# Kernel tuning notes

Hardware: AMD Instinct MI355X
Metric: run time of the kernel (lower is better)

Reference implementation:

```python
import jax, jax.numpy as jnp
import numpy as np

N = 2048   # query length
M = 2048   # key length
B = 2      # batch
D = 1024   # model dim (d_x_q = d_x_kv = d_out)
H = 16     # heads
DQK = D // H
DV = D // H
OFFSET = 0


def setup_inputs() -> dict:
    key = jax.random.key(0)
    k1, k2, k3, k4, k5, k6 = jax.random.split(key, 6)
    return {
        "x_q": jax.random.normal(k1, (N, B, D), dtype=jnp.float32),
        "x_kv": jax.random.normal(k2, (M, B, D), dtype=jnp.float32),
        "to_q": jax.random.normal(k3, (H, DQK, D), dtype=jnp.float32),
        "to_kv": jax.random.normal(k4, (H, DQK + DV, D), dtype=jnp.float32),
        "for_pos_enc": jax.random.normal(k5, (H, DQK, D), dtype=jnp.float32),
        "to_o": jax.random.normal(k6, (D, H, DV), dtype=jnp.float32),
    }


def _pos_enc(for_pos_enc, n, m, offset, d_x_kv):
    # relative distances i - j + offset, range [offset-(m-1), offset+(n-1)]
    dmin = offset - (m - 1)
    dmax = offset + (n - 1)
    r = jnp.arange(dmin, dmax + 1, dtype=jnp.float32)            # [R]
    inv_freq = 1.0 / (10000.0 ** (jnp.arange(0.0, d_x_kv, 2.0, dtype=jnp.float32) / d_x_kv))
    phases = r[:, None] * inv_freq[None, :]                       # [R, d/2]
    sincos = jnp.concatenate([jnp.sin(phases), jnp.cos(phases)], axis=-1)  # [R, d]
    table = jnp.einsum('hdb,rb->rhd', for_pos_enc, sincos)       # [R, H, DQK]
    dists = jnp.arange(n)[:, None] - jnp.arange(m)[None, :] + offset
    return table[dists - dmin]                                    # [n, m, H, DQK]


def reference(x_q, x_kv, to_q, to_kv, for_pos_enc, to_o):
    d_qk = to_q.shape[1]
    q = jnp.einsum('hdb,nzb->nzhd', to_q, x_q)     # [N,B,H,DQK]
    kv = jnp.einsum('hdb,mzb->mzhd', to_kv, x_kv)  # [M,B,H,DQK+DV]
    k = kv[..., :d_qk]
    v = kv[..., d_qk:]
    n, m = x_q.shape[0], x_kv.shape[0]

    pos_enc = _pos_enc(for_pos_enc, n, m, OFFSET, x_kv.shape[-1])

    content_logits = jnp.einsum('nzhd,mzhd->nmzh', q, k)          # [N,M,B,H]
    position_logits = jnp.einsum('nzhd,nmhd->nmzh', q, pos_enc)   # [N,M,B,H]
    logits = content_logits + position_logits

    # causal mask: True above diagonal shifted by 1+offset
    mask = jnp.triu(jnp.ones((n, m), dtype=bool), 1 + OFFSET)
    logits = jnp.where(mask[:, :, None, None], -jnp.inf, logits)

    weights = jax.nn.softmax(logits, axis=1)
    attn = jnp.einsum('nmzh,mzhd->nzhd', weights, v)              # [N,B,H,DV]
    out = jnp.einsum('dhb,nzhb->nzd', to_o, attn)                 # [N,B,D]
    return out
```

## Files before the change

### kernel.cpp

```cpp
#include <hip/hip_runtime.h>
#include <math.h>

#define NQ 2048
#define MKV 2048
#define BZ 2
#define DM 1024
#define NH 16
#define DH 64
#define RTAB 4095
#define R0TAB 1984
#define MTAB (RTAB - R0TAB)
#define LOG2E 1.44269504088896340736f

typedef __bf16 bf16x8 __attribute__((ext_vector_type(8)));
typedef float f32x4 __attribute__((ext_vector_type(4)));

__device__ inline unsigned short f2bf(float x) {
  __bf16 b = (__bf16)x;
  union { __bf16 b; unsigned short u; } v; v.b = b; return v.u;
}
__device__ inline float bf2f(unsigned short h) {
  union { unsigned u; float f; } v; v.u = ((unsigned)h) << 16; return v.f;
}
__device__ inline float fexp2(float x) { return __builtin_amdgcn_exp2f(x); }

#define SWZ(r, b) ((b) ^ (((r) & 7) << 4))
#define VSWZ(dv, m) \
  ((dv) * 128 + (((((m) >> 3) ^ ((dv) & 7) ^ (((dv) >> 3) & 7)) << 4)) + ((m) & 7) * 2)

__device__ inline void gload_lds16(const void* g, void* l) {
  __builtin_amdgcn_global_load_lds((const __attribute__((address_space(1))) void*)g,
                                   (__attribute__((address_space(3))) void*)l, 16, 0, 0);
}

__global__ __launch_bounds__(256) void prep_kernel(
    const float* __restrict__ i0, unsigned short* __restrict__ h0, unsigned short* __restrict__ l0, int n0,
    const float* __restrict__ i1, unsigned short* __restrict__ h1, unsigned short* __restrict__ l1, int n1,
    const float* __restrict__ i2, unsigned short* __restrict__ h2, unsigned short* __restrict__ l2, int n2,
    const float* __restrict__ i3, unsigned short* __restrict__ h3, unsigned short* __restrict__ l3, int n3,
    const float* __restrict__ i4, unsigned short* __restrict__ h4, unsigned short* __restrict__ l4, int n4_,
    const float* __restrict__ i5, unsigned short* __restrict__ h5, unsigned short* __restrict__ l5, int n5,
    unsigned short* __restrict__ schi, unsigned short* __restrict__ sclo) {
  if (blockIdx.y == 6) {
    for (int idx = blockIdx.x * 256 + threadIdx.x; idx < MTAB * DM; idx += gridDim.x * 256) {
      int r = idx / DM;
      int b = idx - r * DM;
      int i = (b < DM / 2) ? b : (b - DM / 2);
      double fr = exp((double)i * (-9.210340371976184 / 512.0));
      float rr = (float)(R0TAB + r - (MKV - 1));
      float ph = rr * (float)fr;
      float val = (b < DM / 2) ? sinf(ph) : cosf(ph);
      unsigned short hb = f2bf(val);
      schi[idx] = hb;
      sclo[idx] = f2bf(val - bf2f(hb));
    }
    return;
  }
  const float* in; unsigned short* hp; unsigned short* lp; int n4;
  switch (blockIdx.y) {
    case 0: in = i0; hp = h0; lp = l0; n4 = n0; break;
    case 1: in = i1; hp = h1; lp = l1; n4 = n1; break;
    case 2: in = i2; hp = h2; lp = l2; n4 = n2; break;
    case 3: in = i3; hp = h3; lp = l3; n4 = n3; break;
    case 4: in = i4; hp = h4; lp = l4; n4 = n4_; break;
    default: in = i5; hp = h5; lp = l5; n4 = n5; break;
  }
  for (int i = blockIdx.x * 256 + threadIdx.x; i < n4; i += gridDim.x * 256) {
    float4 v = ((const float4*)in)[i];
    float f[4] = {v.x, v.y, v.z, v.w};
    ushort4 hq, lq;
    unsigned short* hh = (unsigned short*)&hq;
    unsigned short* ll = (unsigned short*)&lq;
#pragma unroll
    for (int e = 0; e < 4; ++e) {
      unsigned short hb = f2bf(f[e]);
      hh[e] = hb;
      ll[e] = f2bf(f[e] - bf2f(hb));
    }
    ((ushort4*)hp)[i] = hq;
    ((ushort4*)lp)[i] = lq;
  }
}

template <int SPLIT_OUT>
__device__ __forceinline__ void gemm_body(
    const unsigned short* __restrict__ Ahi, const unsigned short* __restrict__ Alo,
    const unsigned short* __restrict__ Bhi, const unsigned short* __restrict__ Blo,
    float* __restrict__ Cf, unsigned short* __restrict__ Chi, unsigned short* __restrict__ Clo,
    int M, int N, int row0, int col0, char* lds, float cscale) {
  const int K = 1024;
  char* sAh = lds;
  char* sAl = lds + 16384;
  char* sBh = lds + 32768;
  char* sBl = lds + 49152;
  const int t = threadIdx.x;
  const int w = t >> 6;
  const int lane = t & 63;
  const int lo = lane & 15;
  const int hi = lane >> 4;
  const int wm = w >> 1, wn = w & 1;

  f32x4 acc[4][4];
#pragma unroll
  for (int a = 0; a < 4; ++a)
#pragma unroll
    for (int b = 0; b < 4; ++b) acc[a][b] = (f32x4){0.f, 0.f, 0.f, 0.f};

  for (int k0 = 0; k0 < K; k0 += 64) {
#pragma unroll
    for (int i = 0; i < 4; ++i) {
      int L = i * 4096 + t * 16;
      int r = L >> 7;
      int c16 = (L >> 4) & 7;
      int g16 = c16 ^ (r & 7);
      int ra = row0 + r;
      if (ra >= M) ra = M - 1;
      int rb = col0 + r;
      const char* gah = (const char*)(Ahi + (size_t)ra * K + k0) + g16 * 16;
      const char* gal = (const char*)(Alo + (size_t)ra * K + k0) + g16 * 16;
      const char* gbh = (const char*)(Bhi + (size_t)rb * K + k0) + g16 * 16;
      const char* gbl = (const char*)(Blo + (size_t)rb * K + k0) + g16 * 16;
      gload_lds16(gah, sAh + L);
      gload_lds16(gal, sAl + L);
      gload_lds16(gbh, sBh + L);
      gload_lds16(gbl, sBl + L);
    }
    __syncthreads();
#pragma unroll
    for (int ks = 0; ks < 2; ++ks) {
      bf16x8 ah[4], al[4], bh[4], bl[4];
#pragma unroll
      for (int f = 0; f < 4; ++f) {
        int rA = wm * 64 + 16 * f + lo;
        int offA = rA * 128 + (((4 * ks + hi) ^ (rA & 7)) << 4);
        ah[f] = *(const bf16x8*)(sAh + offA);
        al[f] = *(const bf16x8*)(sAl + offA);
        int rB = wn * 64 + 16 * f + lo;
        int offB = rB * 128 + (((4 * ks + hi) ^ (rB & 7)) << 4);
        bh[f] = *(const bf16x8*)(sBh + offB);
        bl[f] = *(const bf16x8*)(sBl + offB);
      }
#pragma unroll
      for (int fm = 0; fm < 4; ++fm)
#pragma unroll
        for (int fn = 0; fn < 4; ++fn) {
          acc[fm][fn] = __builtin_amdgcn_mfma_f32_16x16x32_bf16(ah[fm], bh[fn], acc[fm][fn], 0, 0, 0);
          acc[fm][fn] = __builtin_amdgcn_mfma_f32_16x16x32_bf16(ah[fm], bl[fn], acc[fm][fn], 0, 0, 0);
          acc[fm][fn] = __builtin_amdgcn_mfma_f32_16x16x32_bf16(al[fm], bh[fn], acc[fm][fn], 0, 0, 0);
        }
    }
    __syncthreads();
  }
#pragma unroll
  for (int fm = 0; fm < 4; ++fm)
#pragma unroll
    for (int qq = 0; qq < 4; ++qq) {
      int row = row0 + wm * 64 + 16 * fm + 4 * hi + qq;
      if (row < M) {
#pragma unroll
        for (int fn = 0; fn < 4; ++fn) {
          int col = col0 + wn * 64 + 16 * fn + lo;
          float v = acc[fm][fn][qq] * cscale;
          if (SPLIT_OUT) {
            unsigned short hb = f2bf(v);
            Chi[(size_t)row * N + col] = hb;
            Clo[(size_t)row * N + col] = f2bf(v - bf2f(hb));
          } else {
            Cf[(size_t)row * N + col] = v;
          }
        }
      }
    }
}

__global__ __launch_bounds__(256, 2) void gemm3_kernel(
    const unsigned short* __restrict__ xqh, const unsigned short* __restrict__ xql,
    const unsigned short* __restrict__ tqh, const unsigned short* __restrict__ tql,
    unsigned short* __restrict__ qh, unsigned short* __restrict__ ql,
    const unsigned short* __restrict__ xkh, const unsigned short* __restrict__ xkl,
    const unsigned short* __restrict__ tkh, const unsigned short* __restrict__ tkl,
    unsigned short* __restrict__ kvh, unsigned short* __restrict__ kvl,
    const unsigned short* __restrict__ sch, const unsigned short* __restrict__ scl,
    const unsigned short* __restrict__ fph, const unsigned short* __restrict__ fpl,
    unsigned short* __restrict__ tbh, unsigned short* __restrict__ tbl) {
  __shared__ char lds[65536];
  int bx = blockIdx.x;
  if (bx < 256) {
    int gx = bx & 7, gy = bx >> 3;
    gemm_body<1>(xqh, xql, tqh, tql, nullptr, qh, ql, 4096, 1024, gy * 128, gx * 128, lds, LOG2E);
  } else if (bx < 768) {
    bx -= 256;
    int gx = bx & 15, gy = bx >> 4;
    gemm_body<1>(xkh, xkl, tkh, tkl, nullptr, kvh, kvl, 4096, 2048, gy * 128, gx * 128, lds, 1.0f);
  } else {
    bx -= 768;
    int gx = bx & 7, gy = bx >> 3;
    gemm_body<1>(sch, scl, fph, fpl, nullptr, tbh, tbl, MTAB, 1024, gy * 128, gx * 128, lds, 1.0f);
  }
}

__global__ __launch_bounds__(256, 2) void gemm_out_kernel(
    const unsigned short* __restrict__ Ahi, const unsigned short* __restrict__ Alo,
    const unsigned short* __restrict__ Bhi, const unsigned short* __restrict__ Blo,
    float* __restrict__ Cf) {
  __shared__ char lds[65536];
  gemm_body<0>(Ahi, Alo, Bhi, Blo, Cf, nullptr, nullptr, 4096, 1024,
               blockIdx.y * 128, blockIdx.x * 128, lds, 1.0f);
}

union U8 { uint4 q; unsigned short u[8]; };

__global__ __launch_bounds__(256, 2) void attn_kernel(
    const unsigned short* __restrict__ qhi, const unsigned short* __restrict__ qlo,
    const unsigned short* __restrict__ kvhi, const unsigned short* __restrict__ kvlo,
    const unsigned short* __restrict__ tabhi, const unsigned short* __restrict__ tablo,
    unsigned short* __restrict__ ohi, unsigned short* __restrict__ olo) {
  __shared__ __align__(16) char sKhi[8192];
  __shared__ __align__(16) char sKlo[8192];
  __shared__ __align__(16) char sT[32768];
  __shared__ __align__(16) char sVT[8192];
  __shared__ __align__(16) char sP[8192];

  const int t = threadIdx.x;
  const int w = t >> 6;
  const int lane = t & 63;
  const int lo = lane & 15;
  const int hi = lane >> 4;

  for (int rep = 0; rep < 2; ++rep) {
    const int item = rep == 0 ? (1023 - (int)blockIdx.x) : (int)blockIdx.x;
    const int qb = item >> 5;
    const int z = (item >> 4) & 1;
    const int h = item & 15;
    const int n0 = qb * 64;

    bf16x8 qh[2], ql[2];
    {
      size_t qoff = (size_t)((n0 + 16 * w + lo) * BZ + z) * DM + h * DH;
#pragma unroll
      for (int ks = 0; ks < 2; ++ks) {
        qh[ks] = *(const bf16x8*)(qhi + qoff + 32 * ks + 8 * hi);
        ql[ks] = *(const bf16x8*)(qlo + qoff + 32 * ks + 8 * hi);
      }
    }

    f32x4 accO[4];
#pragma unroll
    for (int f = 0; f < 4; ++f) accO[f] = (f32x4){0.f, 0.f, 0.f, 0.f};
    float mi[4], li[4];
#pragma unroll
    for (int qq = 0; qq < 4; ++qq) { mi[qq] = -1e30f; li[qq] = 0.f; }

    uint4 pVh[2];
#pragma unroll
    for (int it = 0; it < 2; ++it) {
      int f = it * 256 + t;
      int j = f >> 3;
      int d8 = (f & 7) << 3;
      size_t gb = (size_t)((0 + j) * BZ + z) * (NH * 2 * DH) + h * (2 * DH);
      pVh[it] = *(const uint4*)(kvhi + gb + DH + d8);
    }

    for (int mt = 0; mt <= qb; ++mt) {
      const int m0 = mt * 64;
      const int Wb = n0 - m0 + R0TAB;
      __syncthreads();

#pragma unroll
      for (int it = 0; it < 2; ++it) {
        int f = it * 256 + t;
        int j = f >> 3;
        int c = f & 7;
        int gsw = (c ^ (j & 7)) << 3;
        size_t gb = (size_t)((m0 + j) * BZ + z) * (NH * 2 * DH) + h * (2 * DH);
        gload_lds16(kvhi + gb + gsw, sKhi + f * 16);
        gload_lds16(kvlo + gb + gsw, sKlo + f * 16);
      }
      if (mt == 0) {
#pragma unroll
        for (int it = 0; it < 4; ++it) {
          int f = it * 256 + t;
          int rr = f >> 3;
          int c = f & 7;
          int g = Wb + rr;
          int gc = g < RTAB ? g : (RTAB - 1);
          int slot = g & 127;
          int gsw = (c ^ (g & 7)) << 3;
          size_t gb = (size_t)gc * DM + h * DH;
          gload_lds16(tabhi + gb + gsw, sT + slot * 128 + c * 16);
          gload_lds16(tablo + gb + gsw, sT + 16384 + slot * 128 + c * 16);
        }
      } else {
#pragma unroll
        for (int it = 0; it < 2; ++it) {
          int f = it * 256 + t;
          int rr = f >> 3;
          int c = f & 7;
          int g = Wb + rr;
          int slot = g & 127;
          int gsw = (c ^ (g & 7)) << 3;
          size_t gb = (size_t)g * DM + h * DH;
          gload_lds16(tabhi + gb + gsw, sT + slot * 128 + c * 16);
          gload_lds16(tablo + gb + gsw, sT + 16384 + slot * 128 + c * 16);
        }
      }

#pragma unroll
      for (int it = 0; it < 2; ++it) {
        int f = it * 256 + t;
        int j = f >> 3;
        int d8 = (f & 7) << 3;
        U8 vh;
        vh.q = pVh[it];
#pragma unroll
        for (int e = 0; e < 8; ++e) {
          int dv = d8 + e;
          *(unsigned short*)(sVT + VSWZ(dv, j)) = vh.u[e];
        }
      }
      if (mt < qb) {
        const int m0n = (mt + 1) * 64;
#pragma unroll
        for (int it = 0; it < 2; ++it) {
          int f = it * 256 + t;
          int j = f >> 3;
          int d8 = (f & 7) << 3;
          size_t gb = (size_t)((m0n + j) * BZ + z) * (NH * 2 * DH) + h * (2 * DH);
          pVh[it] = *(const uint4*)(kvhi + gb + DH + d8);
        }
      }
      __syncthreads();

      f32x4 accS[4], accPL[5];
#pragma unroll
      for (int f = 0; f < 4; ++f) accS[f] = (f32x4){0.f, 0.f, 0.f, 0.f};
#pragma unroll
      for (int f = 0; f < 5; ++f) accPL[f] = (f32x4){0.f, 0.f, 0.f, 0.f};
#pragma unroll
      for (int ks = 0; ks < 2; ++ks) {
#pragma unroll
        for (int fm = 0; fm < 4; ++fm) {
          int rb = SWZ(lo, (16 * fm + lo) * 128 + (32 * ks + 8 * hi) * 2);
          bf16x8 kh = *(const bf16x8*)(sKhi + rb);
          bf16x8 kl = *(const bf16x8*)(sKlo + rb);
          accS[fm] = __builtin_amdgcn_mfma_f32_16x16x32_bf16(qh[ks], kh, accS[fm], 0, 0, 0);
          accS[fm] = __builtin_amdgcn_mfma_f32_16x16x32_bf16(qh[ks], kl, accS[fm], 0, 0, 0);
          accS[fm] = __builtin_amdgcn_mfma_f32_16x16x32_bf16(ql[ks], kh, accS[fm], 0, 0, 0);
        }
#pragma unroll
        for (int fr = 0; fr < 5; ++fr) {
          int g = Wb + 16 * (w + fr) + lo;
          int rb = (g & 127) * 128 + (((4 * ks + hi) ^ (g & 7)) << 4);
          bf16x8 th = *(const bf16x8*)(sT + rb);
          bf16x8 tl = *(const bf16x8*)(sT + 16384 + rb);
          accPL[fr] = __builtin_amdgcn_mfma_f32_16x16x32_bf16(qh[ks], th, accPL[fr], 0, 0, 0);
          accPL[fr] = __builtin_amdgcn_mfma_f32_16x16x32_bf16(qh[ks], tl, accPL[fr], 0, 0, 0);
          accPL[fr] = __builtin_amdgcn_mfma_f32_16x16x32_bf16(ql[ks], th, accPL[fr], 0, 0, 0);
        }
      }

#pragma unroll
      for (int fm = 0; fm < 4; ++fm)
#pragma unroll
        for (int qq = 0; qq < 4; ++qq) {
          int rn = 4 * hi + qq + 63 - 16 * fm - lo;
          float va = __shfl(accPL[3 - fm][qq], rn & 15, 16);
          float vb = __shfl(accPL[4 - fm][qq], rn & 15, 16);
          accS[fm][qq] += (rn >> 4) == (3 - fm) ? va : vb;
        }

      if (mt == qb) {
#pragma unroll
        for (int fm = 0; fm < 4; ++fm)
#pragma unroll
          for (int qq = 0; qq < 4; ++qq)
            if (16 * fm + lo > 16 * w + 4 * hi + qq) accS[fm][qq] = -1e30f;
      }

#pragma unroll
      for (int qq = 0; qq < 4; ++qq) {
        float pm = fmaxf(fmaxf(accS[0][qq], accS[1][qq]), fmaxf(accS[2][qq], accS[3][qq]));
        pm = fmaxf(pm, __shfl_xor(pm, 1));
        pm = fmaxf(pm, __shfl_xor(pm, 2));
        pm = fmaxf(pm, __shfl_xor(pm, 4));
        pm = fmaxf(pm, __shfl_xor(pm, 8));
        float mn = fmaxf(mi[qq], pm);
        float a = fexp2(mi[qq] - mn);
        mi[qq] = mn;
        float rs = 0.f;
#pragma unroll
        for (int fm = 0; fm < 4; ++fm) {
          float p = fexp2(accS[fm][qq] - mn);
          accS[fm][qq] = p;
          rs += p;
        }
        rs += __shfl_xor(rs, 1);
        rs += __shfl_xor(rs, 2);
        rs += __shfl_xor(rs, 4);
        rs += __shfl_xor(rs, 8);
        li[qq] = li[qq] * a + rs;
#pragma unroll
        for (int f = 0; f < 4; ++f) accO[f][qq] *= a;
      }

#pragma unroll
      for (int fm = 0; fm < 4; ++fm)
#pragma unroll
        for (int qq = 0; qq < 4; ++qq) {
          int row = 16 * w + 4 * hi + qq;
          *(unsigned short*)(sP + SWZ(4 * hi + qq, row * 128 + (16 * fm + lo) * 2)) =
              f2bf(accS[fm][qq]);
        }

#pragma unroll
      for (int ks = 0; ks < 2; ++ks) {
        int ab = SWZ(lo, (16 * w + lo) * 128 + (32 * ks + 8 * hi) * 2);
        bf16x8 pa = *(const bf16x8*)(sP + ab);
#pragma unroll
        for (int fv = 0; fv < 4; ++fv) {
          int dv = 16 * fv + lo;
          int vb = dv * 128 + ((((4 * ks + hi) ^ (dv & 7) ^ ((dv >> 3) & 7))) << 4);
          bf16x8 vv = *(const bf16x8*)(sVT + vb);
          accO[fv] = __builtin_amdgcn_mfma_f32_16x16x32_bf16(pa, vv, accO[fv], 0, 0, 0);
        }
      }
    }

#pragma unroll
    for (int qq = 0; qq < 4; ++qq) {
      float inv = 1.0f / li[qq];
      int n = n0 + 16 * w + 4 * hi + qq;
#pragma unroll
      for (int fv = 0; fv < 4; ++fv) {
        size_t idx = (size_t)(n * BZ + z) * DM + h * DH + 16 * fv + lo;
        float v = accO[fv][qq] * inv;
        unsigned short hb = f2bf(v);
        ohi[idx] = hb;
        olo[idx] = f2bf(v - bf2f(hb));
      }
    }
  }
}

extern "C" void kernel_launch(void* const* d_in, const int* in_sizes, int n_in,
                              void* d_out, int out_size, void* d_ws, size_t ws_size,
                              hipStream_t stream) {
  const float* x_q   = (const float*)d_in[0];
  const float* x_kv  = (const float*)d_in[1];
  const float* to_q  = (const float*)d_in[2];
  const float* to_kv = (const float*)d_in[3];
  const float* fpe   = (const float*)d_in[4];
  const float* to_o  = (const float*)d_in[5];
  float* out = (float*)d_out;

  char* W = (char*)d_ws;
  size_t o = 0;
  auto alloc = [&](size_t bytes) { char* p = W + o; o += (bytes + 255) & ~(size_t)255; return p; };
  typedef unsigned short us;
  us* q_hi  = (us*)alloc((size_t)4096 * 1024 * 2);
  us* q_lo  = (us*)alloc((size_t)4096 * 1024 * 2);
  us* kv_hi = (us*)alloc((size_t)4096 * 2048 * 2);
  us* kv_lo = (us*)alloc((size_t)4096 * 2048 * 2);
  us* tab_hi = (us*)alloc((size_t)RTAB * 1024 * 2);
  us* tab_lo = (us*)alloc((size_t)RTAB * 1024 * 2);
  us* xq_hi = (us*)alloc((size_t)4096 * 1024 * 2);
  us* xq_lo = (us*)alloc((size_t)4096 * 1024 * 2);
  us* xkv_hi = (us*)alloc((size_t)4096 * 1024 * 2);
  us* xkv_lo = (us*)alloc((size_t)4096 * 1024 * 2);
  us* tq_hi  = (us*)alloc((size_t)1024 * 1024 * 2);
  us* tq_lo  = (us*)alloc((size_t)1024 * 1024 * 2);
  us* tkv_hi = (us*)alloc((size_t)2048 * 1024 * 2);
  us* tkv_lo = (us*)alloc((size_t)2048 * 1024 * 2);
  us* to_hi  = (us*)alloc((size_t)1024 * 1024 * 2);
  us* to_lo  = (us*)alloc((size_t)1024 * 1024 * 2);
  us* fpe_hi = (us*)alloc((size_t)1024 * 1024 * 2);
  us* fpe_lo = (us*)alloc((size_t)1024 * 1024 * 2);
  us* sc_hi  = (us*)alloc((size_t)MTAB * 1024 * 2);
  us* sc_lo  = (us*)alloc((size_t)MTAB * 1024 * 2);

  prep_kernel<<<dim3(4096, 7), 256, 0, stream>>>(
      x_q,   xq_hi,  xq_lo,  4096 * 1024 / 4,
      x_kv,  xkv_hi, xkv_lo, 4096 * 1024 / 4,
      to_q,  tq_hi,  tq_lo,  1024 * 1024 / 4,
      to_kv, tkv_hi, tkv_lo, 2048 * 1024 / 4,
      to_o,  to_hi,  to_lo,  1024 * 1024 / 4,
      fpe,   fpe_hi, fpe_lo, 1024 * 1024 / 4,
      sc_hi, sc_lo);

  gemm3_kernel<<<dim3(904), 256, 0, stream>>>(
      xq_hi, xq_lo, tq_hi, tq_lo, q_hi, q_lo,
      xkv_hi, xkv_lo, tkv_hi, tkv_lo, kv_hi, kv_lo,
      sc_hi, sc_lo, fpe_hi, fpe_lo,
      tab_hi + (size_t)R0TAB * 1024, tab_lo + (size_t)R0TAB * 1024);

  us* at_hi = xkv_hi;
  us* at_lo = xkv_lo;
  attn_kernel<<<dim3(512), 256, 0, stream>>>(q_hi, q_lo, kv_hi, kv_lo,
                                             tab_hi, tab_lo, at_hi, at_lo);
  gemm_out_kernel<<<dim3(8, 32), 256, 0, stream>>>(at_hi, at_lo, to_hi, to_lo, out);
}
```

Baseline: 266.5 us.

## Drop low-precision split for attention output and V, simplify output GEMM

The attention output is now stored as a single bf16 value instead of a hi/lo pair. The output projection becomes a plain single-bf16 GEMM with 64x128 tiles and more blocks, replacing the three-product split-precision GEMM. The KV projection skips writing the lo half for the V columns. Softmax row reductions use DPP row-rotate moves instead of shuffles. Together these cut output-GEMM compute and memory traffic at the cost of lower accuracy in the V path and the output projection.

```diff
diff --git a/kernel.cpp b/kernel.cpp
--- a/kernel.cpp
+++ b/kernel.cpp
@@ -23,6 +23,28 @@
   union { unsigned u; float f; } v; v.u = ((unsigned)h) << 16; return v.f;
 }
 __device__ inline float fexp2(float x) { return __builtin_amdgcn_exp2f(x); }
+
+template <int N>
+__device__ inline float ror16(float x) {
+  union { float f; int i; } a, r;
+  a.f = x;
+  r.i = __builtin_amdgcn_mov_dpp(a.i, 0x120 | N, 0xf, 0xf, true);
+  return r.f;
+}
+__device__ inline float rowmax16(float x) {
+  x = fmaxf(x, ror16<1>(x));
+  x = fmaxf(x, ror16<2>(x));
+  x = fmaxf(x, ror16<4>(x));
+  x = fmaxf(x, ror16<8>(x));
+  return x;
+}
+__device__ inline float rowsum16(float x) {
+  x += ror16<1>(x);
+  x += ror16<2>(x);
+  x += ror16<4>(x);
+  x += ror16<8>(x);
+  return x;
+}
 
 #define SWZ(r, b) ((b) ^ (((r) & 7) << 4))
 #define VSWZ(dv, m) \
@@ -82,7 +104,7 @@
   }
 }
 
-template <int SPLIT_OUT>
+template <int SPLIT_OUT, int KVSKIP>
 __device__ __forceinline__ void gemm_body(
     const unsigned short* __restrict__ Ahi, const unsigned short* __restrict__ Alo,
     const unsigned short* __restrict__ Bhi, const unsigned short* __restrict__ Blo,
@@ -164,7 +186,8 @@
           if (SPLIT_OUT) {
             unsigned short hb = f2bf(v);
             Chi[(size_t)row * N + col] = hb;
-            Clo[(size_t)row * N + col] = f2bf(v - bf2f(hb));
+            if (!KVSKIP || wn == 0)
+              Clo[(size_t)row * N + col] = f2bf(v - bf2f(hb));
           } else {
             Cf[(size_t)row * N + col] = v;
           }
@@ -187,25 +210,86 @@
   int bx = blockIdx.x;
   if (bx < 256) {
     int gx = bx & 7, gy = bx >> 3;
-    gemm_body<1>(xqh, xql, tqh, tql, nullptr, qh, ql, 4096, 1024, gy * 128, gx * 128, lds, LOG2E);
+    gemm_body<1, 0>(xqh, xql, tqh, tql, nullptr, qh, ql, 4096, 1024, gy * 128, gx * 128, lds, LOG2E);
   } else if (bx < 768) {
     bx -= 256;
     int gx = bx & 15, gy = bx >> 4;
-    gemm_body<1>(xkh, xkl, tkh, tkl, nullptr, kvh, kvl, 4096, 2048, gy * 128, gx * 128, lds, 1.0f);
+    gemm_body<1, 1>(xkh, xkl, tkh, tkl, nullptr, kvh, kvl, 4096, 2048, gy * 128, gx * 128, lds, 1.0f);
   } else {
     bx -= 768;
     int gx = bx & 7, gy = bx >> 3;
-    gemm_body<1>(sch, scl, fph, fpl, nullptr, tbh, tbl, MTAB, 1024, gy * 128, gx * 128, lds, 1.0f);
+    gemm_body<1, 0>(sch, scl, fph, fpl, nullptr, tbh, tbl, MTAB, 1024, gy * 128, gx * 128, lds, 1.0f);
   }
 }
 
 __global__ __launch_bounds__(256, 2) void gemm_out_kernel(
-    const unsigned short* __restrict__ Ahi, const unsigned short* __restrict__ Alo,
-    const unsigned short* __restrict__ Bhi, const unsigned short* __restrict__ Blo,
-    float* __restrict__ Cf) {
-  __shared__ char lds[65536];
-  gemm_body<0>(Ahi, Alo, Bhi, Blo, Cf, nullptr, nullptr, 4096, 1024,
-               blockIdx.y * 128, blockIdx.x * 128, lds, 1.0f);
+    const unsigned short* __restrict__ A,
+    const unsigned short* __restrict__ B,
+    float* __restrict__ C) {
+  __shared__ __align__(16) char sA[8192];
+  __shared__ __align__(16) char sB[16384];
+  const int t = threadIdx.x;
+  const int w = t >> 6;
+  const int lane = t & 63;
+  const int lo = lane & 15;
+  const int hi = lane >> 4;
+  const int row0 = blockIdx.y * 64;
+  const int col0 = blockIdx.x * 128;
+
+  f32x4 acc[4][2];
+#pragma unroll
+  for (int a = 0; a < 4; ++a)
+#pragma unroll
+    for (int b = 0; b < 2; ++b) acc[a][b] = (f32x4){0.f, 0.f, 0.f, 0.f};
+
+  for (int k0 = 0; k0 < 1024; k0 += 64) {
+#pragma unroll
+    for (int it = 0; it < 2; ++it) {
+      int f = it * 256 + t;
+      int r = f >> 3;
+      int c = f & 7;
+      int g16 = c ^ (r & 7);
+      gload_lds16(A + (size_t)(row0 + r) * 1024 + k0 + g16 * 8, sA + f * 16);
+    }
+#pragma unroll
+    for (int it = 0; it < 4; ++it) {
+      int f = it * 256 + t;
+      int r = f >> 3;
+      int c = f & 7;
+      int g16 = c ^ (r & 7);
+      gload_lds16(B + (size_t)(col0 + r) * 1024 + k0 + g16 * 8, sB + f * 16);
+    }
+    __syncthreads();
+#pragma unroll
+    for (int ks = 0; ks < 2; ++ks) {
+      bf16x8 af[4], bf_[2];
+#pragma unroll
+      for (int f = 0; f < 4; ++f) {
+        int rA = 16 * f + lo;
+        af[f] = *(const bf16x8*)(sA + rA * 128 + (((4 * ks + hi) ^ (rA & 7)) << 4));
+      }
+#pragma unroll
+      for (int f = 0; f < 2; ++f) {
+        int rB = 32 * w + 16 * f + lo;
+        bf_[f] = *(const bf16x8*)(sB + rB * 128 + (((4 * ks + hi) ^ (rB & 7)) << 4));
+      }
+#pragma unroll
+      for (int fm = 0; fm < 4; ++fm)
+#pragma unroll
+        for (int fn = 0; fn < 2; ++fn)
+          acc[fm][fn] = __builtin_amdgcn_mfma_f32_16x16x32_bf16(af[fm], bf_[fn], acc[fm][fn], 0, 0, 0);
+    }
+    __syncthreads();
+  }
+#pragma unroll
+  for (int fm = 0; fm < 4; ++fm)
+#pragma unroll
+    for (int qq = 0; qq < 4; ++qq) {
+      int row = row0 + 16 * fm + 4 * hi + qq;
+#pragma unroll
+      for (int fn = 0; fn < 2; ++fn)
+        C[(size_t)row * 1024 + col0 + 32 * w + 16 * fn + lo] = acc[fm][fn][qq];
+    }
 }
 
 union U8 { uint4 q; unsigned short u[8]; };
@@ -214,7 +298,7 @@
     const unsigned short* __restrict__ qhi, const unsigned short* __restrict__ qlo,
     const unsigned short* __restrict__ kvhi, const unsigned short* __restrict__ kvlo,
     const unsigned short* __restrict__ tabhi, const unsigned short* __restrict__ tablo,
-    unsigned short* __restrict__ ohi, unsigned short* __restrict__ olo) {
+    unsigned short* __restrict__ ohi) {
   __shared__ __align__(16) char sKhi[8192];
   __shared__ __align__(16) char sKlo[8192];
   __shared__ __align__(16) char sT[32768];
@@ -380,10 +464,7 @@
 #pragma unroll
       for (int qq = 0; qq < 4; ++qq) {
         float pm = fmaxf(fmaxf(accS[0][qq], accS[1][qq]), fmaxf(accS[2][qq], accS[3][qq]));
-        pm = fmaxf(pm, __shfl_xor(pm, 1));
-        pm = fmaxf(pm, __shfl_xor(pm, 2));
-        pm = fmaxf(pm, __shfl_xor(pm, 4));
-        pm = fmaxf(pm, __shfl_xor(pm, 8));
+        pm = rowmax16(pm);
         float mn = fmaxf(mi[qq], pm);
         float a = fexp2(mi[qq] - mn);
         mi[qq] = mn;
@@ -394,10 +475,7 @@
           accS[fm][qq] = p;
           rs += p;
         }
-        rs += __shfl_xor(rs, 1);
-        rs += __shfl_xor(rs, 2);
-        rs += __shfl_xor(rs, 4);
-        rs += __shfl_xor(rs, 8);
+        rs = rowsum16(rs);
         li[qq] = li[qq] * a + rs;
 #pragma unroll
         for (int f = 0; f < 4; ++f) accO[f][qq] *= a;
@@ -433,10 +511,7 @@
 #pragma unroll
       for (int fv = 0; fv < 4; ++fv) {
         size_t idx = (size_t)(n * BZ + z) * DM + h * DH + 16 * fv + lo;
-        float v = accO[fv][qq] * inv;
-        unsigned short hb = f2bf(v);
-        ohi[idx] = hb;
-        olo[idx] = f2bf(v - bf2f(hb));
+        ohi[idx] = f2bf(accO[fv][qq] * inv);
       }
     }
   }
@@ -494,8 +569,7 @@
       tab_hi + (size_t)R0TAB * 1024, tab_lo + (size_t)R0TAB * 1024);
 
   us* at_hi = xkv_hi;
-  us* at_lo = xkv_lo;
   attn_kernel<<<dim3(512), 256, 0, stream>>>(q_hi, q_lo, kv_hi, kv_lo,
-                                             tab_hi, tab_lo, at_hi, at_lo);
-  gemm_out_kernel<<<dim3(8, 32), 256, 0, stream>>>(at_hi, at_lo, to_hi, to_lo, out);
-}
+                                             tab_hi, tab_lo, at_hi);
+  gemm_out_kernel<<<dim3(8, 64), 256, 0, stream>>>(at_hi, to_hi, out);
+}
```

Result: faster. 234.0 us (-12.2%).
